# Optimization experiments

Measured on AMD Instinct MI355X. Metric: run time of the kernel, lower is better.

Reference implementation:

```python
import jax, jax.numpy as jnp
import numpy as np

KVOL = 8  # kernel volume of a 2x2x2 transposed conv in 3D


def _tconv(y, T, parent, offset):
    # y: [M, C] coarse features, T: [KVOL, C, D] tconv kernel
    # Each coarse voxel emits KVOL candidate outputs; each existing fine voxel
    # gathers from its unique (parent, offset) pair (gather-GEMM form of
    # MinkowskiConvolutionTranspose with kernel=2, stride=2).
    z = jnp.einsum('mc,kcd->mkd', y, T)  # [M, KVOL, D]
    return z[parent, offset]             # [N_fine, D]


def setup_inputs() -> dict:
    key = jax.random.key(0)
    ks = jax.random.split(key, 12)
    N1, N2, N3 = 400000, 120000, 30000
    C1, C2, C3, D = 64, 128, 256, 128
    inp = {
        'feats1': jax.random.normal(ks[0], (N1, C1), jnp.float32),
        'feats2': jax.random.normal(ks[1], (N2, C2), jnp.float32),
        'feats3': jax.random.normal(ks[2], (N3, C3), jnp.float32),
        'parent1': jax.random.randint(ks[3], (N1,), 0, N2, jnp.int32),
        'offset1': jax.random.randint(ks[4], (N1,), 0, KVOL, jnp.int32),
        'parent2': jax.random.randint(ks[5], (N2,), 0, N3, jnp.int32),
        'offset2': jax.random.randint(ks[6], (N2,), 0, KVOL, jnp.int32),
        'W1': jax.random.normal(ks[7], (C1, D), jnp.float32) * 0.05,
        'W2': jax.random.normal(ks[8], (C2, D), jnp.float32) * 0.05,
        'W3': jax.random.normal(ks[9], (C3, D), jnp.float32) * 0.05,
        'T2': jax.random.normal(ks[10], (KVOL, D, D), jnp.float32) * 0.05,
        'T3': jax.random.normal(ks[11], (KVOL, D, D), jnp.float32) * 0.05,
    }
    return inp


def reference(feats1, feats2, feats3, parent1, offset1, parent2, offset2,
              W1, W2, W3, T2, T3):
    # Top-down FPN merge: start at coarsest level (3), upsample, add skips.
    y = feats3 @ W3                                   # conv1x1['3']
    y = _tconv(y, T3, parent2, offset2) + feats2 @ W2  # tconv['3'] + conv1x1['2']
    y = _tconv(y, T2, parent1, offset1) + feats1 @ W1  # tconv['2'] + conv1x1['1']
    return y  # [N1, out_channels]
```

## Files before the change

### kernel.cpp

```cpp
#include <hip/hip_runtime.h>

typedef __bf16 v8bf __attribute__((ext_vector_type(8)));
typedef float  v4f  __attribute__((ext_vector_type(4)));

__device__ inline unsigned pack_bf16x2(float x, float y) {
    unsigned short a = __builtin_bit_cast(unsigned short, (__bf16)x);
    unsigned short b = __builtin_bit_cast(unsigned short, (__bf16)y);
    return (unsigned)a | ((unsigned)b << 16);
}


__global__ void pack_weights(const float* __restrict__ W1, const float* __restrict__ W2,
                             const float* __restrict__ W3, const float* __restrict__ T2,
                             const float* __restrict__ T3,
                             __bf16* __restrict__ W3T, __bf16* __restrict__ BT3,
                             __bf16* __restrict__ BT2) {
    int idx = blockIdx.x * 256 + threadIdx.x;
    if (idx < 32768) {
        int c = idx & 255, d = idx >> 8;
        W3T[d * 256 + c] = (__bf16)W3[c * 128 + d];
    } else if (idx < 32768 + 262144) {
        int t = idx - 32768;
        int c = t & 255, rest = t >> 8;
        int d = rest & 127, k = rest >> 7;
        float v = (c < 128) ? T3[((k * 128 + c) * 128) + d] : W2[(c - 128) * 128 + d];
        BT3[t] = (__bf16)v;
    } else if (idx < 32768 + 262144 + 196608) {
        int t = idx - (32768 + 262144);
        int c = t % 192, rest = t / 192;
        int d = rest & 127, k = rest >> 7;
        float v = (c < 128) ? T2[((k * 128 + c) * 128) + d] : W1[(c - 128) * 128 + d];
        BT2[t] = (__bf16)v;
    }
}

__global__ void hist_kernel(const int* __restrict__ off1, int n1,
                            const int* __restrict__ off2, int n2, int* __restrict__ ctr) {
    __shared__ int lh[16];
    if (threadIdx.x < 16) lh[threadIdx.x] = 0;
    __syncthreads();
    int total = n1 + n2;
    for (int idx = blockIdx.x * blockDim.x + threadIdx.x; idx < total;
         idx += gridDim.x * blockDim.x) {
        if (idx < n1) atomicAdd(&lh[off1[idx]], 1);
        else          atomicAdd(&lh[8 + off2[idx - n1]], 1);
    }
    __syncthreads();
    if (threadIdx.x < 16) atomicAdd(&ctr[threadIdx.x], lh[threadIdx.x]);
}

__global__ void scan_kernel(int* ctr) {
    if (threadIdx.x == 0 && blockIdx.x == 0) {
        int s = 0, tb = 0;
        for (int g = 0; g < 8; ++g) {
            ctr[32 + g] = s; ctr[16 + g] = s; ctr[50 + g] = tb;
            s += ctr[g]; tb += (ctr[g] + 63) >> 6;
        }
        ctr[32 + 8] = s; ctr[50 + 8] = tb;
        s = 0; tb = 0;
        for (int g = 0; g < 8; ++g) {
            ctr[41 + g] = s; ctr[24 + g] = s; ctr[59 + g] = tb;
            s += ctr[8 + g]; tb += (ctr[8 + g] + 63) >> 6;
        }
        ctr[41 + 8] = s; ctr[59 + 8] = tb;
    }
}

__global__ void scatter_kernel(const int* __restrict__ off1, int n1, int nb1,
                               const int* __restrict__ off2, int n2,
                               int* __restrict__ ctr, int* __restrict__ perm1,
                               int* __restrict__ perm2) {
    __shared__ int lh[8], gb[8];
    const int* off; int n, base; int* cursor; int* perm;
    if ((int)blockIdx.x < nb1) {
        off = off1; n = n1; base = blockIdx.x * 1024; cursor = ctr + 16; perm = perm1;
    } else {
        off = off2; n = n2; base = (blockIdx.x - nb1) * 1024; cursor = ctr + 24; perm = perm2;
    }
    if (threadIdx.x < 8) lh[threadIdx.x] = 0;
    __syncthreads();
    for (int rr = 0; rr < 4; ++rr) {
        int i = base + rr * 256 + (int)threadIdx.x;
        int o = -1, rank = 0;
        if (i < n) { o = off[i]; rank = atomicAdd(&lh[o], 1); }
        __syncthreads();
        if (threadIdx.x < 8) {
            int c = lh[threadIdx.x];
            gb[threadIdx.x] = c ? atomicAdd(&cursor[threadIdx.x], c) : 0;
        }
        __syncthreads();
        if (o >= 0) perm[gb[o] + rank] = i;
        __syncthreads();
        if (threadIdx.x < 8) lh[threadIdx.x] = 0;
        __syncthreads();
    }
}

template <int K, int CP, int CS, bool GATHER, bool OUT_BF16>
__global__ __launch_bounds__(256, 1) void gemm_k(
    const float* __restrict__ Askip, const __bf16* __restrict__ Aprev,
    const __bf16* __restrict__ BT, const int* __restrict__ perm,
    const int* __restrict__ parent, const int* __restrict__ ctr,
    int gs_off, int tb_off, void* __restrict__ outp, int M) {
    constexpr int LD = K + 8;
    __shared__ __align__(16) __bf16 Al[64 * LD];
    __shared__ __align__(16) __bf16 Bl[128 * LD];
    __shared__ int orow[64];

    int g, r0, mcount;
    if constexpr (GATHER) {
        const int* tb = ctr + tb_off;
        int b = blockIdx.x;
        if (b >= tb[8]) return;
        g = 0;
        while (b >= tb[g + 1]) ++g;
        const int* gs = ctr + gs_off;
        r0 = gs[g] + (b - tb[g]) * 64;
        mcount = min(64, gs[g + 1] - r0);
    } else {
        g = 0;
        r0 = blockIdx.x * 64;
        mcount = min(64, M - r0);
    }

    const int tid = threadIdx.x;
    {
        int j = tid >> 2, part = tid & 3;
        if (j < mcount) {
            int i, p = 0;
            if constexpr (GATHER) { i = perm[r0 + j]; p = parent[i]; }
            else { i = r0 + j; }
            if (part == 0) orow[j] = i;
            __bf16* arow = &Al[j * LD];
            if constexpr (CP > 0) {
                const uint4* src = (const uint4*)(Aprev + (size_t)p * CP) + part * (CP / 32);
                uint4* dst = (uint4*)arow + part * (CP / 32);
#pragma unroll
                for (int v = 0; v < CP / 32; ++v) dst[v] = src[v];
            }
            {
                const float4* src = (const float4*)(Askip + (size_t)i * CS) + part * (CS / 16);
                uint4* dst = (uint4*)(arow + CP + part * (CS / 4));
#pragma unroll
                for (int v = 0; v < CS / 16; v += 2) {
                    float4 f0 = src[v], f1 = src[v + 1];
                    uint4 w;
                    w.x = pack_bf16x2(f0.x, f0.y);
                    w.y = pack_bf16x2(f0.z, f0.w);
                    w.z = pack_bf16x2(f1.x, f1.y);
                    w.w = pack_bf16x2(f1.z, f1.w);
                    dst[v / 2] = w;
                }
            }
        }
    }
    {
        int n = tid >> 1, half = tid & 1;
        const uint4* src = (const uint4*)(BT + ((size_t)g * 128 + n) * K) + half * (K / 16);
        uint4* dst = (uint4*)(Bl + n * LD) + half * (K / 16);
#pragma unroll
        for (int v = 0; v < K / 16; ++v) dst[v] = src[v];
    }
    __syncthreads();

    const int lane = tid & 63;
    const int wv = tid >> 6;
    const int m = lane & 15;
    const int q = lane >> 4;
    v4f acc[8] = {};
    const __bf16* arow = &Al[(wv * 16 + m) * LD + q * 8];
    const __bf16* brow = &Bl[m * LD + q * 8];
#pragma unroll
    for (int kk = 0; kk < K; kk += 32) {
        v8bf a = *(const v8bf*)(arow + kk);
#pragma unroll
        for (int t = 0; t < 8; ++t) {
            v8bf b = *(const v8bf*)(brow + t * 16 * LD + kk);
            acc[t] = __builtin_amdgcn_mfma_f32_16x16x32_bf16(a, b, acc[t], 0, 0, 0);
        }
    }

#pragma unroll
    for (int r = 0; r < 4; ++r) {
        int j = wv * 16 + q * 4 + r;
        if (j < mcount) {
            size_t row = (size_t)orow[j] * 128;
            if constexpr (OUT_BF16) {
                __bf16* out = (__bf16*)outp;
#pragma unroll
                for (int t = 0; t < 8; ++t) out[row + t * 16 + m] = (__bf16)acc[t][r];
            } else {
                float* out = (float*)outp;
#pragma unroll
                for (int t = 0; t < 8; ++t) out[row + t * 16 + m] = acc[t][r];
            }
        }
    }
}

extern "C" void kernel_launch(void* const* d_in, const int* in_sizes, int n_in,
                              void* d_out, int out_size, void* d_ws, size_t ws_size,
                              hipStream_t stream) {
    const float* feats1 = (const float*)d_in[0];
    const float* feats2 = (const float*)d_in[1];
    const float* feats3 = (const float*)d_in[2];
    const int* parent1 = (const int*)d_in[3];
    const int* offset1 = (const int*)d_in[4];
    const int* parent2 = (const int*)d_in[5];
    const int* offset2 = (const int*)d_in[6];
    const float* W1 = (const float*)d_in[7];
    const float* W2 = (const float*)d_in[8];
    const float* W3 = (const float*)d_in[9];
    const float* T2 = (const float*)d_in[10];
    const float* T3 = (const float*)d_in[11];
    const int N1 = in_sizes[0] / 64;
    const int N2 = in_sizes[1] / 128;
    const int N3 = in_sizes[2] / 256;

    char* p = (char*)d_ws;
    auto take = [&](size_t bytes) {
        char* r = p;
        p += (bytes + 255) & ~(size_t)255;
        return r;
    };
    __bf16* y3b = (__bf16*)take((size_t)N3 * 128 * 2);
    __bf16* y2b = (__bf16*)take((size_t)N2 * 128 * 2);
    __bf16* W3T = (__bf16*)take((size_t)32768 * 2);
    __bf16* BT3 = (__bf16*)take((size_t)262144 * 2);
    __bf16* BT2 = (__bf16*)take((size_t)196608 * 2);
    int* perm1 = (int*)take((size_t)N1 * 4);
    int* perm2 = (int*)take((size_t)N2 * 4);
    int* ctr = (int*)take(68 * 4);

    hipMemsetAsync(ctr, 0, 16 * 4, stream);
    pack_weights<<<1920, 256, 0, stream>>>(W1, W2, W3, T2, T3, W3T, BT3, BT2);
    hist_kernel<<<512, 256, 0, stream>>>(offset1, N1, offset2, N2, ctr);
    scan_kernel<<<1, 64, 0, stream>>>(ctr);
    int nb1 = (N1 + 1023) / 1024, nb2 = (N2 + 1023) / 1024;
    scatter_kernel<<<nb1 + nb2, 256, 0, stream>>>(offset1, N1, nb1, offset2, N2, ctr, perm1,
                                                  perm2);
    gemm_k<256, 0, 256, false, true><<<(N3 + 63) / 64, 256, 0, stream>>>(
        feats3, nullptr, W3T, nullptr, nullptr, nullptr, 0, 0, y3b, N3);
    gemm_k<256, 128, 128, true, true><<<(N2 + 63) / 64 + 8, 256, 0, stream>>>(
        feats2, y3b, BT3, perm2, parent2, ctr, 41, 59, y2b, N2);
    gemm_k<192, 128, 64, true, false><<<(N1 + 63) / 64 + 8, 256, 0, stream>>>(
        feats1, y2b, BT2, perm1, parent1, ctr, 32, 50, d_out, N1);
}
```

Measured before the change: 483.3 us.

## Hold weight fragments in registers and split GEMM output columns per wave

The GEMM kernel no longer stages the 128xK weight tile in LDS. Each wave loads its own 32-column slice of B directly from global memory into registers, and every wave computes all 64 rows for those columns. This cuts LDS use per block, so launch bounds now ask for 3 blocks per CU to raise occupancy, but it puts more pressure on registers. The weight-packing and histogram kernels are also merged into one launch to save a kernel launch.

```diff
diff --git a/kernel.cpp b/kernel.cpp
--- a/kernel.cpp
+++ b/kernel.cpp
@@ -10,43 +10,46 @@
 }
 
 
-__global__ void pack_weights(const float* __restrict__ W1, const float* __restrict__ W2,
-                             const float* __restrict__ W3, const float* __restrict__ T2,
-                             const float* __restrict__ T3,
-                             __bf16* __restrict__ W3T, __bf16* __restrict__ BT3,
-                             __bf16* __restrict__ BT2) {
-    int idx = blockIdx.x * 256 + threadIdx.x;
-    if (idx < 32768) {
-        int c = idx & 255, d = idx >> 8;
-        W3T[d * 256 + c] = (__bf16)W3[c * 128 + d];
-    } else if (idx < 32768 + 262144) {
-        int t = idx - 32768;
-        int c = t & 255, rest = t >> 8;
-        int d = rest & 127, k = rest >> 7;
-        float v = (c < 128) ? T3[((k * 128 + c) * 128) + d] : W2[(c - 128) * 128 + d];
-        BT3[t] = (__bf16)v;
-    } else if (idx < 32768 + 262144 + 196608) {
-        int t = idx - (32768 + 262144);
-        int c = t % 192, rest = t / 192;
-        int d = rest & 127, k = rest >> 7;
-        float v = (c < 128) ? T2[((k * 128 + c) * 128) + d] : W1[(c - 128) * 128 + d];
-        BT2[t] = (__bf16)v;
-    }
-}
-
-__global__ void hist_kernel(const int* __restrict__ off1, int n1,
-                            const int* __restrict__ off2, int n2, int* __restrict__ ctr) {
-    __shared__ int lh[16];
-    if (threadIdx.x < 16) lh[threadIdx.x] = 0;
-    __syncthreads();
-    int total = n1 + n2;
-    for (int idx = blockIdx.x * blockDim.x + threadIdx.x; idx < total;
-         idx += gridDim.x * blockDim.x) {
-        if (idx < n1) atomicAdd(&lh[off1[idx]], 1);
-        else          atomicAdd(&lh[8 + off2[idx - n1]], 1);
-    }
-    __syncthreads();
-    if (threadIdx.x < 16) atomicAdd(&ctr[threadIdx.x], lh[threadIdx.x]);
+__global__ void pack_hist(const float* __restrict__ W1, const float* __restrict__ W2,
+                          const float* __restrict__ W3, const float* __restrict__ T2,
+                          const float* __restrict__ T3,
+                          __bf16* __restrict__ W3T, __bf16* __restrict__ BT3,
+                          __bf16* __restrict__ BT2,
+                          const int* __restrict__ off1, int n1,
+                          const int* __restrict__ off2, int n2, int* __restrict__ ctr) {
+    if (blockIdx.x < 1920) {
+        int idx = blockIdx.x * 256 + threadIdx.x;
+        if (idx < 32768) {
+            int c = idx & 255, d = idx >> 8;
+            W3T[d * 256 + c] = (__bf16)W3[c * 128 + d];
+        } else if (idx < 32768 + 262144) {
+            int t = idx - 32768;
+            int c = t & 255, rest = t >> 8;
+            int d = rest & 127, k = rest >> 7;
+            float v = (c < 128) ? T3[((k * 128 + c) * 128) + d] : W2[(c - 128) * 128 + d];
+            BT3[t] = (__bf16)v;
+        } else if (idx < 32768 + 262144 + 196608) {
+            int t = idx - (32768 + 262144);
+            int c = t % 192, rest = t / 192;
+            int d = rest & 127, k = rest >> 7;
+            float v = (c < 128) ? T2[((k * 128 + c) * 128) + d] : W1[(c - 128) * 128 + d];
+            BT2[t] = (__bf16)v;
+        }
+    } else {
+        __shared__ int lh[16];
+        if (threadIdx.x < 16) lh[threadIdx.x] = 0;
+        __syncthreads();
+        int total = n1 + n2;
+        for (int idx = (blockIdx.x - 1920) * 256 + threadIdx.x; idx < total; idx += 512 * 256) {
+            if (idx < n1) atomicAdd(&lh[off1[idx]], 1);
+            else          atomicAdd(&lh[8 + off2[idx - n1]], 1);
+        }
+        __syncthreads();
+        if (threadIdx.x < 16) {
+            int c = lh[threadIdx.x];
+            if (c) atomicAdd(&ctr[threadIdx.x], c);
+        }
+    }
 }
 
 __global__ void scan_kernel(int* ctr) {
@@ -96,15 +99,14 @@
     }
 }
 
-template <int K, int CP, int CS, bool GATHER, bool OUT_BF16>
-__global__ __launch_bounds__(256, 1) void gemm_k(
+template <int K, int CP, int CS, bool GATHER, bool OUT_BF16, int MINW>
+__global__ __launch_bounds__(256, MINW) void gemm_k(
     const float* __restrict__ Askip, const __bf16* __restrict__ Aprev,
     const __bf16* __restrict__ BT, const int* __restrict__ perm,
     const int* __restrict__ parent, const int* __restrict__ ctr,
     int gs_off, int tb_off, void* __restrict__ outp, int M) {
     constexpr int LD = K + 8;
     __shared__ __align__(16) __bf16 Al[64 * LD];
-    __shared__ __align__(16) __bf16 Bl[128 * LD];
     __shared__ int orow[64];
 
     int g, r0, mcount;
@@ -124,6 +126,22 @@
     }
 
     const int tid = threadIdx.x;
+    const int lane = tid & 63;
+    const int w = tid >> 6;
+    const int m = lane & 15;
+    const int q = lane >> 4;
+
+    constexpr int KS = K / 32;
+    v8bf bfrag[2][KS];
+    {
+        const __bf16* bbase = BT + ((size_t)g * 128 + w * 32 + m) * K + q * 8;
+#pragma unroll
+        for (int t = 0; t < 2; ++t)
+#pragma unroll
+            for (int kk = 0; kk < KS; ++kk)
+                bfrag[t][kk] = *(const v8bf*)(bbase + (size_t)t * 16 * K + kk * 32);
+    }
+
     {
         int j = tid >> 2, part = tid & 3;
         if (j < mcount) {
@@ -144,55 +162,45 @@
 #pragma unroll
                 for (int v = 0; v < CS / 16; v += 2) {
                     float4 f0 = src[v], f1 = src[v + 1];
-                    uint4 w;
-                    w.x = pack_bf16x2(f0.x, f0.y);
-                    w.y = pack_bf16x2(f0.z, f0.w);
-                    w.z = pack_bf16x2(f1.x, f1.y);
-                    w.w = pack_bf16x2(f1.z, f1.w);
-                    dst[v / 2] = w;
+                    uint4 wd;
+                    wd.x = pack_bf16x2(f0.x, f0.y);
+                    wd.y = pack_bf16x2(f0.z, f0.w);
+                    wd.z = pack_bf16x2(f1.x, f1.y);
+                    wd.w = pack_bf16x2(f1.z, f1.w);
+                    dst[v / 2] = wd;
                 }
             }
         }
     }
-    {
-        int n = tid >> 1, half = tid & 1;
-        const uint4* src = (const uint4*)(BT + ((size_t)g * 128 + n) * K) + half * (K / 16);
-        uint4* dst = (uint4*)(Bl + n * LD) + half * (K / 16);
-#pragma unroll
-        for (int v = 0; v < K / 16; ++v) dst[v] = src[v];
-    }
     __syncthreads();
 
-    const int lane = tid & 63;
-    const int wv = tid >> 6;
-    const int m = lane & 15;
-    const int q = lane >> 4;
-    v4f acc[8] = {};
-    const __bf16* arow = &Al[(wv * 16 + m) * LD + q * 8];
-    const __bf16* brow = &Bl[m * LD + q * 8];
-#pragma unroll
-    for (int kk = 0; kk < K; kk += 32) {
-        v8bf a = *(const v8bf*)(arow + kk);
-#pragma unroll
-        for (int t = 0; t < 8; ++t) {
-            v8bf b = *(const v8bf*)(brow + t * 16 * LD + kk);
-            acc[t] = __builtin_amdgcn_mfma_f32_16x16x32_bf16(a, b, acc[t], 0, 0, 0);
-        }
-    }
-
-#pragma unroll
-    for (int r = 0; r < 4; ++r) {
-        int j = wv * 16 + q * 4 + r;
-        if (j < mcount) {
-            size_t row = (size_t)orow[j] * 128;
-            if constexpr (OUT_BF16) {
-                __bf16* out = (__bf16*)outp;
-#pragma unroll
-                for (int t = 0; t < 8; ++t) out[row + t * 16 + m] = (__bf16)acc[t][r];
-            } else {
-                float* out = (float*)outp;
-#pragma unroll
-                for (int t = 0; t < 8; ++t) out[row + t * 16 + m] = acc[t][r];
+    v4f acc[4][2] = {};
+#pragma unroll
+    for (int kk = 0; kk < KS; ++kk) {
+#pragma unroll
+        for (int rt = 0; rt < 4; ++rt) {
+            v8bf a = *(const v8bf*)(&Al[(rt * 16 + m) * LD + q * 8 + kk * 32]);
+            acc[rt][0] = __builtin_amdgcn_mfma_f32_16x16x32_bf16(a, bfrag[0][kk], acc[rt][0], 0, 0, 0);
+            acc[rt][1] = __builtin_amdgcn_mfma_f32_16x16x32_bf16(a, bfrag[1][kk], acc[rt][1], 0, 0, 0);
+        }
+    }
+
+#pragma unroll
+    for (int rt = 0; rt < 4; ++rt) {
+#pragma unroll
+        for (int r = 0; r < 4; ++r) {
+            int j = rt * 16 + q * 4 + r;
+            if (j < mcount) {
+                size_t row = (size_t)orow[j] * 128 + w * 32;
+                if constexpr (OUT_BF16) {
+                    __bf16* out = (__bf16*)outp;
+                    out[row + m]      = (__bf16)acc[rt][0][r];
+                    out[row + 16 + m] = (__bf16)acc[rt][1][r];
+                } else {
+                    float* out = (float*)outp;
+                    out[row + m]      = acc[rt][0][r];
+                    out[row + 16 + m] = acc[rt][1][r];
+                }
             }
         }
     }
@@ -233,16 +241,16 @@
     int* ctr = (int*)take(68 * 4);
 
     hipMemsetAsync(ctr, 0, 16 * 4, stream);
-    pack_weights<<<1920, 256, 0, stream>>>(W1, W2, W3, T2, T3, W3T, BT3, BT2);
-    hist_kernel<<<512, 256, 0, stream>>>(offset1, N1, offset2, N2, ctr);
+    pack_hist<<<2432, 256, 0, stream>>>(W1, W2, W3, T2, T3, W3T, BT3, BT2,
+                                        offset1, N1, offset2, N2, ctr);
     scan_kernel<<<1, 64, 0, stream>>>(ctr);
     int nb1 = (N1 + 1023) / 1024, nb2 = (N2 + 1023) / 1024;
     scatter_kernel<<<nb1 + nb2, 256, 0, stream>>>(offset1, N1, nb1, offset2, N2, ctr, perm1,
                                                   perm2);
-    gemm_k<256, 0, 256, false, true><<<(N3 + 63) / 64, 256, 0, stream>>>(
+    gemm_k<256, 0, 256, false, true, 3><<<(N3 + 63) / 64, 256, 0, stream>>>(
         feats3, nullptr, W3T, nullptr, nullptr, nullptr, 0, 0, y3b, N3);
-    gemm_k<256, 128, 128, true, true><<<(N2 + 63) / 64 + 8, 256, 0, stream>>>(
+    gemm_k<256, 128, 128, true, true, 3><<<(N2 + 63) / 64 + 8, 256, 0, stream>>>(
         feats2, y3b, BT3, perm2, parent2, ctr, 41, 59, y2b, N2);
-    gemm_k<192, 128, 64, true, false><<<(N1 + 63) / 64 + 8, 256, 0, stream>>>(
+    gemm_k<192, 128, 64, true, false, 3><<<(N1 + 63) / 64 + 8, 256, 0, stream>>>(
         feats1, y2b, BT2, perm1, parent1, ctr, 32, 50, d_out, N1);
 }
```

New measurement: 475.4 us. Within noise of the previous version (-1.6%).
